# Kernel optimization log

Measured on AMD Instinct MI355X. Metric: run time of the kernel, lower is better.

## Reference

```python
import jax, jax.numpy as jnp
import numpy as np

N_NODES = 2048
DEG = 16
D = 4
E = N_NODES * DEG          # undirected edge count
TWO_E = 2 * E


def setup_inputs() -> dict:
    key = jax.random.key(0)
    # unique off-diagonal (row, col) pairs: sample from n*(n-1) index space
    rng = np.random.default_rng(0)
    p = rng.choice(N_NODES * (N_NODES - 1), size=E, replace=False)
    row = p // (N_NODES - 1)
    c = p % (N_NODES - 1)
    col = c + (c >= row)  # skip the diagonal -> no self loops, all pairs unique
    # edge_index: first E are (i->j), second E the reversed (j->i) in same order
    edge_index = jnp.asarray(
        np.stack([np.concatenate([row, col]), np.concatenate([col, row])]),
        dtype=jnp.int64 if jax.config.jax_enable_x64 else jnp.int32,
    )
    maps = jax.random.normal(key, (TWO_E, D, D), dtype=jnp.float32)
    return {"maps": maps, "edge_index": edge_index, "num_nodes": N_NODES}


def reference(maps, edge_index, num_nodes):
    n = num_nodes
    d = maps.shape[1]
    twoE = maps.shape[0]
    e = twoE // 2

    row_all = edge_index[0]
    # R^T R per directed edge  [2E, d, d]
    diag_contrib = jnp.einsum('eki,ekj->eij', maps, maps)
    # scatter-accumulate into per-node diagonal blocks  [n, d, d]
    maps_diag = jax.ops.segment_sum(diag_contrib, row_all, num_segments=n)

    row = edge_index[0, :e]
    col = edge_index[1, :e]
    # R_ij^T R_ji per undirected edge  [E, d, d]
    maps_triu = jnp.einsum('eki,ekj->eij', maps[:e], maps[e:])

    # eval-mode augmentation: identity
    to_inv = maps_diag + jnp.eye(d, dtype=maps.dtype)
    evals, evecs = jnp.linalg.eigh(to_inv)
    inv_root = jnp.clip(evals, 1e-8, None) ** -0.5
    # V diag(l^-1/2) V^T  [n, d, d]
    inv_sqrt = jnp.einsum('nik,nk,njk->nij', evecs, inv_root, evecs)

    maps_triu = inv_sqrt[row] @ maps_triu @ inv_sqrt[col]
    maps_diag = inv_sqrt @ maps_diag @ inv_sqrt
    maps_triu = jnp.clip(maps_triu, -1.0, 1.0)
    maps_diag = jnp.clip(maps_diag, -1.0, 1.0)

    # dense block Laplacian  [n, n, d, d] -> [n*d, n*d]
    L = jnp.zeros((n, n, d, d), dtype=maps.dtype)
    idx = jnp.arange(n)
    L = L.at[idx, idx].set(maps_diag)
    L = L.at[row, col].set(-maps_triu)
    L = L.at[col, row].set(-jnp.swapaxes(maps_triu, 1, 2))
    return L.transpose(0, 2, 1, 3).reshape(n * d, n * d)
```

## Files before the change

kernel.cpp:

```cpp
#include <hip/hip_runtime.h>
#include <math.h>


#define NNODES 2048
#define MAXDEG 96
#define BLK 256

typedef float vfloat4 __attribute__((ext_vector_type(4)));

__global__ void build_lists_kernel(const int* __restrict__ ei,
                                   int* __restrict__ lists,
                                   int* __restrict__ cnts,
                                   int E, int twoE) {
    int e = blockIdx.x * blockDim.x + threadIdx.x;
    if (e >= twoE) return;
    int node = ei[e];
    int nbr = ei[twoE + e];
    int t = (e >= E) ? 1 : 0;
    int u = t ? (e - E) : e;
    int slot = atomicAdd(&cnts[node], 1);
    if (slot < MAXDEG)
        lists[(size_t)node * MAXDEG + slot] = (nbr << 20) | (t << 19) | u;
}

template <int P, int Q>
__device__ __forceinline__ void jrot(float a[4][4], float v[4][4]) {
    float apq = a[P][Q];
    if (fabsf(apq) < 1e-12f) return;
    float theta = (a[Q][Q] - a[P][P]) / (2.0f * apq);
    float t = 1.0f / (fabsf(theta) + sqrtf(theta * theta + 1.0f));
    t = (theta < 0.0f) ? -t : t;
    float c = 1.0f / sqrtf(t * t + 1.0f);
    float s = t * c;
    #pragma unroll
    for (int k = 0; k < 4; ++k) {
        float akp = a[k][P], akq = a[k][Q];
        a[k][P] = c * akp - s * akq;
        a[k][Q] = s * akp + c * akq;
    }
    #pragma unroll
    for (int k = 0; k < 4; ++k) {
        float apk = a[P][k], aqk = a[Q][k];
        a[P][k] = c * apk - s * aqk;
        a[Q][k] = s * apk + c * aqk;
    }
    #pragma unroll
    for (int k = 0; k < 4; ++k) {
        float vkp = v[k][P], vkq = v[k][Q];
        v[k][P] = c * vkp - s * vkq;
        v[k][Q] = s * vkp + c * vkq;
    }
}

__global__ void __launch_bounds__(64)
node_kernel(const float* __restrict__ maps,
            const int* __restrict__ lists,
            const int* __restrict__ cnts,
            float* __restrict__ Smat,
            float* __restrict__ vdiag,
            int E, int n) {
    int node = blockIdx.x * blockDim.x + threadIdx.x;
    if (node >= n) return;
    float gm[4][4];
    #pragma unroll
    for (int i = 0; i < 4; ++i)
        #pragma unroll
        for (int j = 0; j < 4; ++j) gm[i][j] = 0.0f;
    int cnt = cnts[node];
    if (cnt > MAXDEG) cnt = MAXDEG;
    const int* myl = lists + (size_t)node * MAXDEG;
    #pragma unroll 4
    for (int j = 0; j < cnt; ++j) {
        int entry = myl[j];
        int t = (entry >> 19) & 1;
        int u = entry & 0x7FFF;
        int e = t ? (E + u) : u;
        const float4* mp = reinterpret_cast<const float4*>(maps + (size_t)e * 16);
        float4 q0 = mp[0], q1 = mp[1], q2 = mp[2], q3 = mp[3];
        float m[4][4] = {{q0.x, q0.y, q0.z, q0.w}, {q1.x, q1.y, q1.z, q1.w},
                         {q2.x, q2.y, q2.z, q2.w}, {q3.x, q3.y, q3.z, q3.w}};
        #pragma unroll
        for (int i = 0; i < 4; ++i)
            #pragma unroll
            for (int jj = 0; jj < 4; ++jj)
                gm[i][jj] += m[0][i] * m[0][jj] + m[1][i] * m[1][jj] +
                             m[2][i] * m[2][jj] + m[3][i] * m[3][jj];
    }
    float a[4][4], v[4][4];
    #pragma unroll
    for (int i = 0; i < 4; ++i)
        #pragma unroll
        for (int j = 0; j < 4; ++j) {
            a[i][j] = gm[i][j] + (i == j ? 1.0f : 0.0f);
            v[i][j] = (i == j) ? 1.0f : 0.0f;
        }
    #pragma unroll
    for (int sweep = 0; sweep < 6; ++sweep) {
        jrot<0, 1>(a, v); jrot<0, 2>(a, v); jrot<0, 3>(a, v);
        jrot<1, 2>(a, v); jrot<1, 3>(a, v); jrot<2, 3>(a, v);
    }
    float ir[4];
    #pragma unroll
    for (int m = 0; m < 4; ++m)
        ir[m] = 1.0f / sqrtf(fmaxf(a[m][m], 1e-8f));
    float s[4][4];
    #pragma unroll
    for (int i = 0; i < 4; ++i)
        #pragma unroll
        for (int j = 0; j < 4; ++j)
            s[i][j] = v[i][0] * v[j][0] * ir[0] + v[i][1] * v[j][1] * ir[1] +
                      v[i][2] * v[j][2] * ir[2] + v[i][3] * v[j][3] * ir[3];
    float4* sp = reinterpret_cast<float4*>(Smat + (size_t)node * 16);
    sp[0] = make_float4(s[0][0], s[0][1], s[0][2], s[0][3]);
    sp[1] = make_float4(s[1][0], s[1][1], s[1][2], s[1][3]);
    sp[2] = make_float4(s[2][0], s[2][1], s[2][2], s[2][3]);
    sp[3] = make_float4(s[3][0], s[3][1], s[3][2], s[3][3]);
    float t1[4][4];
    #pragma unroll
    for (int i = 0; i < 4; ++i)
        #pragma unroll
        for (int j = 0; j < 4; ++j)
            t1[i][j] = s[i][0] * gm[0][j] + s[i][1] * gm[1][j] +
                       s[i][2] * gm[2][j] + s[i][3] * gm[3][j];
    float4* vp = reinterpret_cast<float4*>(vdiag + (size_t)node * 16);
    #pragma unroll
    for (int i = 0; i < 4; ++i) {
        float r0 = t1[i][0] * s[0][0] + t1[i][1] * s[1][0] + t1[i][2] * s[2][0] + t1[i][3] * s[3][0];
        float r1 = t1[i][0] * s[0][1] + t1[i][1] * s[1][1] + t1[i][2] * s[2][1] + t1[i][3] * s[3][1];
        float r2 = t1[i][0] * s[0][2] + t1[i][1] * s[1][2] + t1[i][2] * s[2][2] + t1[i][3] * s[3][2];
        float r3 = t1[i][0] * s[0][3] + t1[i][1] * s[1][3] + t1[i][2] * s[2][3] + t1[i][3] * s[3][3];
        vp[i] = make_float4(fminf(fmaxf(r0, -1.0f), 1.0f),
                            fminf(fmaxf(r1, -1.0f), 1.0f),
                            fminf(fmaxf(r2, -1.0f), 1.0f),
                            fminf(fmaxf(r3, -1.0f), 1.0f));
    }
}

__global__ void __launch_bounds__(BLK)
writer_kernel(const float* __restrict__ maps,
              const int* __restrict__ lists,
              const int* __restrict__ cnts,
              const float* __restrict__ Smat,
              const float* __restrict__ vdiag,
              float* __restrict__ out, int E, int ld) {
    int r = blockIdx.x;
    int tid = threadIdx.x;
    __shared__ int colmap[NNODES];
    __shared__ vfloat4 s_dat[MAXDEG + 1][4];
    for (int i = tid; i < NNODES; i += BLK) colmap[i] = -1;

    int cnt = cnts[r];
    if (cnt > MAXDEG) cnt = MAXDEG;
    int col = -1, t = 0;
    if (tid < cnt) {
        int entry = lists[(size_t)r * MAXDEG + tid];
        col = entry >> 20;
        t = (entry >> 19) & 1;
        int u = entry & 0x7FFF;
        const float4* ap = reinterpret_cast<const float4*>(maps + (size_t)u * 16);
        const float4* bp = reinterpret_cast<const float4*>(maps + (size_t)(E + u) * 16);
        float4 a0 = ap[0], a1 = ap[1], a2 = ap[2], a3 = ap[3];
        float4 b0 = bp[0], b1 = bp[1], b2 = bp[2], b3 = bp[3];
        float A[4][4] = {{a0.x, a0.y, a0.z, a0.w}, {a1.x, a1.y, a1.z, a1.w},
                         {a2.x, a2.y, a2.z, a2.w}, {a3.x, a3.y, a3.z, a3.w}};
        float B[4][4] = {{b0.x, b0.y, b0.z, b0.w}, {b1.x, b1.y, b1.z, b1.w},
                         {b2.x, b2.y, b2.z, b2.w}, {b3.x, b3.y, b3.z, b3.w}};
        float C[4][4];
        #pragma unroll
        for (int i = 0; i < 4; ++i)
            #pragma unroll
            for (int j = 0; j < 4; ++j)
                C[i][j] = A[0][i] * B[0][j] + A[1][i] * B[1][j] +
                          A[2][i] * B[2][j] + A[3][i] * B[3][j];
        int rn = t ? col : r;
        int cn = t ? r : col;
        const float4* srp = reinterpret_cast<const float4*>(Smat + (size_t)rn * 16);
        const float4* scp = reinterpret_cast<const float4*>(Smat + (size_t)cn * 16);
        float4 s0 = srp[0], s1 = srp[1], s2 = srp[2], s3 = srp[3];
        float Sr[4][4] = {{s0.x, s0.y, s0.z, s0.w}, {s1.x, s1.y, s1.z, s1.w},
                          {s2.x, s2.y, s2.z, s2.w}, {s3.x, s3.y, s3.z, s3.w}};
        float4 c0 = scp[0], c1 = scp[1], c2 = scp[2], c3 = scp[3];
        float Sc[4][4] = {{c0.x, c0.y, c0.z, c0.w}, {c1.x, c1.y, c1.z, c1.w},
                          {c2.x, c2.y, c2.z, c2.w}, {c3.x, c3.y, c3.z, c3.w}};
        float t1m[4][4];
        #pragma unroll
        for (int i = 0; i < 4; ++i)
            #pragma unroll
            for (int j = 0; j < 4; ++j)
                t1m[i][j] = Sr[i][0] * C[0][j] + Sr[i][1] * C[1][j] +
                            Sr[i][2] * C[2][j] + Sr[i][3] * C[3][j];
        float W[4][4];
        #pragma unroll
        for (int i = 0; i < 4; ++i)
            #pragma unroll
            for (int j = 0; j < 4; ++j) {
                float x = t1m[i][0] * Sc[0][j] + t1m[i][1] * Sc[1][j] +
                          t1m[i][2] * Sc[2][j] + t1m[i][3] * Sc[3][j];
                W[i][j] = -fminf(fmaxf(x, -1.0f), 1.0f);
            }
        if (t) {
            s_dat[tid][0] = (vfloat4){W[0][0], W[1][0], W[2][0], W[3][0]};
            s_dat[tid][1] = (vfloat4){W[0][1], W[1][1], W[2][1], W[3][1]};
            s_dat[tid][2] = (vfloat4){W[0][2], W[1][2], W[2][2], W[3][2]};
            s_dat[tid][3] = (vfloat4){W[0][3], W[1][3], W[2][3], W[3][3]};
        } else {
            s_dat[tid][0] = (vfloat4){W[0][0], W[0][1], W[0][2], W[0][3]};
            s_dat[tid][1] = (vfloat4){W[1][0], W[1][1], W[1][2], W[1][3]};
            s_dat[tid][2] = (vfloat4){W[2][0], W[2][1], W[2][2], W[2][3]};
            s_dat[tid][3] = (vfloat4){W[3][0], W[3][1], W[3][2], W[3][3]};
        }
    }
    if (tid < 4) {
        float4 dv = reinterpret_cast<const float4*>(vdiag + (size_t)r * 16)[tid];
        s_dat[MAXDEG][tid] = (vfloat4){dv.x, dv.y, dv.z, dv.w};
    }
    __syncthreads();
    if (tid < cnt && !t) colmap[col] = tid;
    __syncthreads();
    if (tid < cnt && t) colmap[col] = tid;
    if (tid == 0) colmap[r] = MAXDEG;
    __syncthreads();

    size_t base = (size_t)(r * 4) * (size_t)ld;
    const vfloat4 zero = (vfloat4){0.f, 0.f, 0.f, 0.f};
    #pragma unroll
    for (int ri = 0; ri < 4; ++ri) {
        vfloat4* orow = reinterpret_cast<vfloat4*>(out + base + (size_t)ri * ld);
        for (int cb = tid; cb < NNODES; cb += BLK) {
            int sl = colmap[cb];
            vfloat4 val = zero;
            if (sl >= 0) val = s_dat[sl][ri];
            __builtin_nontemporal_store(val, &orow[cb]);
        }
    }
}

extern "C" void kernel_launch(void* const* d_in, const int* in_sizes, int n_in,
                              void* d_out, int out_size, void* d_ws, size_t ws_size,
                              hipStream_t stream) {
    const float* maps = (const float*)d_in[0];
    const int* ei = (const int*)d_in[1];
    int twoE = in_sizes[0] / 16;
    int E = twoE / 2;
    int n = NNODES;
    int ld = n * 4;
    float* out = (float*)d_out;

    int*   ws_cnt  = (int*)d_ws;
    int*   ws_list = ws_cnt + n;
    float* ws_S    = (float*)(ws_list + (size_t)n * MAXDEG);
    float* ws_vd   = ws_S + (size_t)n * 16;

    (void)hipMemsetAsync(ws_cnt, 0, (size_t)n * sizeof(int), stream);
    build_lists_kernel<<<(twoE + BLK - 1) / BLK, BLK, 0, stream>>>(
        ei, ws_list, ws_cnt, E, twoE);
    node_kernel<<<(n + 63) / 64, 64, 0, stream>>>(
        maps, ws_list, ws_cnt, ws_S, ws_vd, E, n);
    writer_kernel<<<n, BLK, 0, stream>>>(
        maps, ws_list, ws_cnt, ws_S, ws_vd, out, E, ld);
}
```

Before: 107.3 us.

## Replace row-writer kernel with memset plus per-edge scatter of off-diagonal blocks

Drops the per-row writer kernel that built a column map in shared memory and streamed every output row, and zeroes the whole dense output with hipMemsetAsync instead. The node kernel now writes each diagonal block straight into the output, and two scatter passes over undirected edges compute the off-diagonal block once per edge and write it and its transpose. This swaps a gather-based full-matrix write for a bulk memset plus scattered 64-byte row stores. Running the two passes in order keeps the reference's rule that the (col,row) write wins when an edge appears in both directions.

```diff
diff --git a/kernel.cpp b/kernel.cpp
--- a/kernel.cpp
+++ b/kernel.cpp
@@ -5,8 +5,6 @@
 #define NNODES 2048
 #define MAXDEG 96
 #define BLK 256
-
-typedef float vfloat4 __attribute__((ext_vector_type(4)));
 
 __global__ void build_lists_kernel(const int* __restrict__ ei,
                                    int* __restrict__ lists,
@@ -57,8 +55,8 @@
             const int* __restrict__ lists,
             const int* __restrict__ cnts,
             float* __restrict__ Smat,
-            float* __restrict__ vdiag,
-            int E, int n) {
+            float* __restrict__ out,
+            int E, int n, int ld) {
     int node = blockIdx.x * blockDim.x + threadIdx.x;
     if (node >= n) return;
     float gm[4][4];
@@ -122,116 +120,82 @@
         for (int j = 0; j < 4; ++j)
             t1[i][j] = s[i][0] * gm[0][j] + s[i][1] * gm[1][j] +
                        s[i][2] * gm[2][j] + s[i][3] * gm[3][j];
-    float4* vp = reinterpret_cast<float4*>(vdiag + (size_t)node * 16);
+    size_t base = ((size_t)node * 4) * (size_t)ld + (size_t)node * 4;
     #pragma unroll
     for (int i = 0; i < 4; ++i) {
         float r0 = t1[i][0] * s[0][0] + t1[i][1] * s[1][0] + t1[i][2] * s[2][0] + t1[i][3] * s[3][0];
         float r1 = t1[i][0] * s[0][1] + t1[i][1] * s[1][1] + t1[i][2] * s[2][1] + t1[i][3] * s[3][1];
         float r2 = t1[i][0] * s[0][2] + t1[i][1] * s[1][2] + t1[i][2] * s[2][2] + t1[i][3] * s[3][2];
         float r3 = t1[i][0] * s[0][3] + t1[i][1] * s[1][3] + t1[i][2] * s[2][3] + t1[i][3] * s[3][3];
-        vp[i] = make_float4(fminf(fmaxf(r0, -1.0f), 1.0f),
-                            fminf(fmaxf(r1, -1.0f), 1.0f),
-                            fminf(fmaxf(r2, -1.0f), 1.0f),
-                            fminf(fmaxf(r3, -1.0f), 1.0f));
-    }
-}
-
-__global__ void __launch_bounds__(BLK)
-writer_kernel(const float* __restrict__ maps,
-              const int* __restrict__ lists,
-              const int* __restrict__ cnts,
-              const float* __restrict__ Smat,
-              const float* __restrict__ vdiag,
-              float* __restrict__ out, int E, int ld) {
-    int r = blockIdx.x;
-    int tid = threadIdx.x;
-    __shared__ int colmap[NNODES];
-    __shared__ vfloat4 s_dat[MAXDEG + 1][4];
-    for (int i = tid; i < NNODES; i += BLK) colmap[i] = -1;
-
-    int cnt = cnts[r];
-    if (cnt > MAXDEG) cnt = MAXDEG;
-    int col = -1, t = 0;
-    if (tid < cnt) {
-        int entry = lists[(size_t)r * MAXDEG + tid];
-        col = entry >> 20;
-        t = (entry >> 19) & 1;
-        int u = entry & 0x7FFF;
-        const float4* ap = reinterpret_cast<const float4*>(maps + (size_t)u * 16);
-        const float4* bp = reinterpret_cast<const float4*>(maps + (size_t)(E + u) * 16);
-        float4 a0 = ap[0], a1 = ap[1], a2 = ap[2], a3 = ap[3];
-        float4 b0 = bp[0], b1 = bp[1], b2 = bp[2], b3 = bp[3];
-        float A[4][4] = {{a0.x, a0.y, a0.z, a0.w}, {a1.x, a1.y, a1.z, a1.w},
-                         {a2.x, a2.y, a2.z, a2.w}, {a3.x, a3.y, a3.z, a3.w}};
-        float B[4][4] = {{b0.x, b0.y, b0.z, b0.w}, {b1.x, b1.y, b1.z, b1.w},
-                         {b2.x, b2.y, b2.z, b2.w}, {b3.x, b3.y, b3.z, b3.w}};
-        float C[4][4];
+        *reinterpret_cast<float4*>(out + base + (size_t)i * ld) =
+            make_float4(fminf(fmaxf(r0, -1.0f), 1.0f),
+                        fminf(fmaxf(r1, -1.0f), 1.0f),
+                        fminf(fmaxf(r2, -1.0f), 1.0f),
+                        fminf(fmaxf(r3, -1.0f), 1.0f));
+    }
+}
+
+template <int PASS>
+__global__ void scatter_kernel(const float* __restrict__ maps,
+                               const int* __restrict__ ei,
+                               const float* __restrict__ Smat,
+                               float* __restrict__ out,
+                               int E, int twoE, int ld) {
+    int u = blockIdx.x * blockDim.x + threadIdx.x;
+    if (u >= E) return;
+    int r = ei[u];
+    int c = ei[twoE + u];
+    const float4* ap = reinterpret_cast<const float4*>(maps + (size_t)u * 16);
+    const float4* bp = reinterpret_cast<const float4*>(maps + (size_t)(E + u) * 16);
+    float4 a0 = ap[0], a1 = ap[1], a2 = ap[2], a3 = ap[3];
+    float4 b0 = bp[0], b1 = bp[1], b2 = bp[2], b3 = bp[3];
+    float A[4][4] = {{a0.x, a0.y, a0.z, a0.w}, {a1.x, a1.y, a1.z, a1.w},
+                     {a2.x, a2.y, a2.z, a2.w}, {a3.x, a3.y, a3.z, a3.w}};
+    float B[4][4] = {{b0.x, b0.y, b0.z, b0.w}, {b1.x, b1.y, b1.z, b1.w},
+                     {b2.x, b2.y, b2.z, b2.w}, {b3.x, b3.y, b3.z, b3.w}};
+    float C[4][4];
+    #pragma unroll
+    for (int i = 0; i < 4; ++i)
+        #pragma unroll
+        for (int j = 0; j < 4; ++j)
+            C[i][j] = A[0][i] * B[0][j] + A[1][i] * B[1][j] +
+                      A[2][i] * B[2][j] + A[3][i] * B[3][j];
+    const float4* srp = reinterpret_cast<const float4*>(Smat + (size_t)r * 16);
+    const float4* scp = reinterpret_cast<const float4*>(Smat + (size_t)c * 16);
+    float4 s0 = srp[0], s1 = srp[1], s2 = srp[2], s3 = srp[3];
+    float Sr[4][4] = {{s0.x, s0.y, s0.z, s0.w}, {s1.x, s1.y, s1.z, s1.w},
+                      {s2.x, s2.y, s2.z, s2.w}, {s3.x, s3.y, s3.z, s3.w}};
+    float4 c0 = scp[0], c1 = scp[1], c2 = scp[2], c3 = scp[3];
+    float Sc[4][4] = {{c0.x, c0.y, c0.z, c0.w}, {c1.x, c1.y, c1.z, c1.w},
+                      {c2.x, c2.y, c2.z, c2.w}, {c3.x, c3.y, c3.z, c3.w}};
+    float t1m[4][4];
+    #pragma unroll
+    for (int i = 0; i < 4; ++i)
+        #pragma unroll
+        for (int j = 0; j < 4; ++j)
+            t1m[i][j] = Sr[i][0] * C[0][j] + Sr[i][1] * C[1][j] +
+                        Sr[i][2] * C[2][j] + Sr[i][3] * C[3][j];
+    float W[4][4];
+    #pragma unroll
+    for (int i = 0; i < 4; ++i)
+        #pragma unroll
+        for (int j = 0; j < 4; ++j) {
+            float x = t1m[i][0] * Sc[0][j] + t1m[i][1] * Sc[1][j] +
+                      t1m[i][2] * Sc[2][j] + t1m[i][3] * Sc[3][j];
+            W[i][j] = -fminf(fmaxf(x, -1.0f), 1.0f);
+        }
+    if (PASS == 0) {
+        size_t base = ((size_t)r * 4) * (size_t)ld + (size_t)c * 4;
         #pragma unroll
         for (int i = 0; i < 4; ++i)
-            #pragma unroll
-            for (int j = 0; j < 4; ++j)
-                C[i][j] = A[0][i] * B[0][j] + A[1][i] * B[1][j] +
-                          A[2][i] * B[2][j] + A[3][i] * B[3][j];
-        int rn = t ? col : r;
-        int cn = t ? r : col;
-        const float4* srp = reinterpret_cast<const float4*>(Smat + (size_t)rn * 16);
-        const float4* scp = reinterpret_cast<const float4*>(Smat + (size_t)cn * 16);
-        float4 s0 = srp[0], s1 = srp[1], s2 = srp[2], s3 = srp[3];
-        float Sr[4][4] = {{s0.x, s0.y, s0.z, s0.w}, {s1.x, s1.y, s1.z, s1.w},
-                          {s2.x, s2.y, s2.z, s2.w}, {s3.x, s3.y, s3.z, s3.w}};
-        float4 c0 = scp[0], c1 = scp[1], c2 = scp[2], c3 = scp[3];
-        float Sc[4][4] = {{c0.x, c0.y, c0.z, c0.w}, {c1.x, c1.y, c1.z, c1.w},
-                          {c2.x, c2.y, c2.z, c2.w}, {c3.x, c3.y, c3.z, c3.w}};
-        float t1m[4][4];
+            *reinterpret_cast<float4*>(out + base + (size_t)i * ld) =
+                make_float4(W[i][0], W[i][1], W[i][2], W[i][3]);
+    } else {
+        size_t base = ((size_t)c * 4) * (size_t)ld + (size_t)r * 4;
         #pragma unroll
         for (int i = 0; i < 4; ++i)
-            #pragma unroll
-            for (int j = 0; j < 4; ++j)
-                t1m[i][j] = Sr[i][0] * C[0][j] + Sr[i][1] * C[1][j] +
-                            Sr[i][2] * C[2][j] + Sr[i][3] * C[3][j];
-        float W[4][4];
-        #pragma unroll
-        for (int i = 0; i < 4; ++i)
-            #pragma unroll
-            for (int j = 0; j < 4; ++j) {
-                float x = t1m[i][0] * Sc[0][j] + t1m[i][1] * Sc[1][j] +
-                          t1m[i][2] * Sc[2][j] + t1m[i][3] * Sc[3][j];
-                W[i][j] = -fminf(fmaxf(x, -1.0f), 1.0f);
-            }
-        if (t) {
-            s_dat[tid][0] = (vfloat4){W[0][0], W[1][0], W[2][0], W[3][0]};
-            s_dat[tid][1] = (vfloat4){W[0][1], W[1][1], W[2][1], W[3][1]};
-            s_dat[tid][2] = (vfloat4){W[0][2], W[1][2], W[2][2], W[3][2]};
-            s_dat[tid][3] = (vfloat4){W[0][3], W[1][3], W[2][3], W[3][3]};
-        } else {
-            s_dat[tid][0] = (vfloat4){W[0][0], W[0][1], W[0][2], W[0][3]};
-            s_dat[tid][1] = (vfloat4){W[1][0], W[1][1], W[1][2], W[1][3]};
-            s_dat[tid][2] = (vfloat4){W[2][0], W[2][1], W[2][2], W[2][3]};
-            s_dat[tid][3] = (vfloat4){W[3][0], W[3][1], W[3][2], W[3][3]};
-        }
-    }
-    if (tid < 4) {
-        float4 dv = reinterpret_cast<const float4*>(vdiag + (size_t)r * 16)[tid];
-        s_dat[MAXDEG][tid] = (vfloat4){dv.x, dv.y, dv.z, dv.w};
-    }
-    __syncthreads();
-    if (tid < cnt && !t) colmap[col] = tid;
-    __syncthreads();
-    if (tid < cnt && t) colmap[col] = tid;
-    if (tid == 0) colmap[r] = MAXDEG;
-    __syncthreads();
-
-    size_t base = (size_t)(r * 4) * (size_t)ld;
-    const vfloat4 zero = (vfloat4){0.f, 0.f, 0.f, 0.f};
-    #pragma unroll
-    for (int ri = 0; ri < 4; ++ri) {
-        vfloat4* orow = reinterpret_cast<vfloat4*>(out + base + (size_t)ri * ld);
-        for (int cb = tid; cb < NNODES; cb += BLK) {
-            int sl = colmap[cb];
-            vfloat4 val = zero;
-            if (sl >= 0) val = s_dat[sl][ri];
-            __builtin_nontemporal_store(val, &orow[cb]);
-        }
+            *reinterpret_cast<float4*>(out + base + (size_t)i * ld) =
+                make_float4(W[0][i], W[1][i], W[2][i], W[3][i]);
     }
 }
 
@@ -249,13 +213,16 @@
     int*   ws_cnt  = (int*)d_ws;
     int*   ws_list = ws_cnt + n;
     float* ws_S    = (float*)(ws_list + (size_t)n * MAXDEG);
-    float* ws_vd   = ws_S + (size_t)n * 16;
-
+
+    (void)hipMemsetAsync(out, 0, (size_t)out_size * sizeof(float), stream);
     (void)hipMemsetAsync(ws_cnt, 0, (size_t)n * sizeof(int), stream);
+
     build_lists_kernel<<<(twoE + BLK - 1) / BLK, BLK, 0, stream>>>(
         ei, ws_list, ws_cnt, E, twoE);
     node_kernel<<<(n + 63) / 64, 64, 0, stream>>>(
-        maps, ws_list, ws_cnt, ws_S, ws_vd, E, n);
-    writer_kernel<<<n, BLK, 0, stream>>>(
-        maps, ws_list, ws_cnt, ws_S, ws_vd, out, E, ld);
-}
+        maps, ws_list, ws_cnt, ws_S, out, E, n, ld);
+    scatter_kernel<0><<<(E + BLK - 1) / BLK, BLK, 0, stream>>>(
+        maps, ei, ws_S, out, E, twoE, ld);
+    scatter_kernel<1><<<(E + BLK - 1) / BLK, BLK, 0, stream>>>(
+        maps, ei, ws_S, out, E, twoE, ld);
+}
```

After: 102.1 us. 4.8% less time.
